# Kernel optimization log

Measured on AMD Instinct MI355X. Metric: run time of the kernel, lower is better.

The kernel has to match this reference:

```python
import jax, jax.numpy as jnp
import numpy as np

N = 50000   # nodes
E = 800000  # edges per relation (avg degree 16)
IN = 128    # input feature dim
H = 2       # attention heads per layer
OUT = 64    # output feats per head
R = 2       # number of relations
NEG_SLOPE = 0.2


def _edge_softmax(e, dst, n):
    # e: [E, H] edge scores; softmax over incoming edges of each dst node
    m = jax.ops.segment_max(e, dst, num_segments=n)  # [N, H]
    m = jnp.where(jnp.isfinite(m), m, 0.0)
    ex = jnp.exp(e - jax.lax.stop_gradient(m)[dst])
    s = jax.ops.segment_sum(ex, dst, num_segments=n)  # [N, H]
    return ex / s[dst]


def _gat_layer(h, W, al, ar, b, src, dst):
    # h: [N, in]; W: [R, in, H*OUT]; al/ar: [R, H, OUT]; b: [R, H*OUT]
    # src/dst: [R, E] int32. HeteroGraphConv with sum aggregation over relations.
    acc = jnp.zeros((N, H, OUT), h.dtype)
    for r in range(R):  # small fixed relation count
        f = (h @ W[r]).reshape(N, H, OUT)           # projected feats
        el = (f * al[r]).sum(-1)                    # [N, H]
        er = (f * ar[r]).sum(-1)                    # [N, H]
        e = jax.nn.leaky_relu(el[src[r]] + er[dst[r]], NEG_SLOPE)  # [E, H]
        a = _edge_softmax(e, dst[r], N)             # [E, H]
        msg = f[src[r]] * a[:, :, None]             # [E, H, OUT]
        agg = jax.ops.segment_sum(msg, dst[r], num_segments=N)     # [N, H, OUT]
        acc = acc + jax.nn.elu(agg + b[r].reshape(1, H, OUT))
    return acc.reshape(N, H * OUT)  # flatten(1)


def setup_inputs() -> dict:
    key = jax.random.key(0)
    k = jax.random.split(key, 13)
    s = 0.05
    f32 = jnp.float32
    return {
        "x": jax.random.normal(k[0], (N, IN), f32),
        "W0": jax.random.normal(k[1], (R, IN, H * OUT), f32) * s,
        "al0": jax.random.normal(k[2], (R, H, OUT), f32) * s,
        "ar0": jax.random.normal(k[3], (R, H, OUT), f32) * s,
        "b0": jax.random.normal(k[4], (R, H * OUT), f32) * s,
        "W1": jax.random.normal(k[5], (R, H * OUT, H * OUT), f32) * s,
        "al1": jax.random.normal(k[6], (R, H, OUT), f32) * s,
        "ar1": jax.random.normal(k[7], (R, H, OUT), f32) * s,
        "b1": jax.random.normal(k[8], (R, H * OUT), f32) * s,
        "src0": jax.random.randint(k[9], (R, E), 0, N, jnp.int32),
        "dst0": jax.random.randint(k[10], (R, E), 0, N, jnp.int32),
        "src1": jax.random.randint(k[11], (R, E), 0, N, jnp.int32),
        "dst1": jax.random.randint(k[12], (R, E), 0, N, jnp.int32),
    }


def reference(x, W0, al0, ar0, b0, W1, al1, ar1, b1, src0, dst0, src1, dst1):
    h = _gat_layer(x, W0, al0, ar0, b0, src0, dst0)  # [N, H*OUT]
    h = _gat_layer(h, W1, al1, ar1, b1, src1, dst1)  # [N, H*OUT]
    return h
```

## Files before the change

kernel.cpp:

```cpp
#include <hip/hip_runtime.h>

#define NN 50000
#define NE 800000
#define DIM 128
#define NB 128
#define CH 4096
#define CAP 8192

typedef unsigned int uint;
typedef unsigned short ushort;
typedef __attribute__((ext_vector_type(8))) short v8s;
typedef __attribute__((ext_vector_type(4))) float v4f;

__device__ __forceinline__ ushort f2bf(float f) {
    union { float f; uint i; } c; c.f = f;
    const uint r = (c.i + 0x7fffu + ((c.i >> 16) & 1u)) >> 16;
    return (ushort)r;
}

__global__ __launch_bounds__(256) void conv_wt(
    const float* __restrict__ W0, const float* __restrict__ W1,
    ushort* __restrict__ WT, int* __restrict__ gcur)
{
    if (blockIdx.x == 64) {
        const int t = threadIdx.x;
        gcur[t] = t * CAP;
        gcur[t + 256] = (t + 256) * CAP;
        return;
    }
    const int t = blockIdx.x * 256 + threadIdx.x;
#pragma unroll
    for (int i = 0; i < 4; i++) {
        const int o = t * 4 + i;
        const int m = o >> 14, rem = o & 16383;
        const int nrow = rem >> 7, k = rem & 127;
        const float* src = (m < 2) ? (W0 + (size_t)m * 16384)
                                   : (W1 + (size_t)(m - 2) * 16384);
        WT[o] = f2bf(src[k * 128 + nrow]);
    }
}

__global__ __launch_bounds__(256) void gemm_dual(
    const ushort* __restrict__ hbf, const float* __restrict__ xf,
    const ushort* __restrict__ WT,
    const float* __restrict__ al, const float* __restrict__ ar,
    ushort* __restrict__ fg0, ushort* __restrict__ fg1,
    float* __restrict__ elb, int n, int is_f32)
{
    __shared__ ushort tile[64][136];
    const int tid = threadIdx.x;
    const int w = tid >> 6, lane = tid & 63;
    const int quad = lane >> 4, l16 = lane & 15;
    const int row0 = blockIdx.x * 64 + w * 16;

    int arow = row0 + l16;
    if (arow >= n) arow = n - 1;

    v8s afr[4];
    if (is_f32) {
        const float* ap = xf + (size_t)arow * DIM + quad * 8;
#pragma unroll
        for (int kt = 0; kt < 4; kt++) {
            const float4 a0 = *(const float4*)(ap + kt * 32);
            const float4 a1 = *(const float4*)(ap + kt * 32 + 4);
            ushort tmp[8] = { f2bf(a0.x), f2bf(a0.y), f2bf(a0.z), f2bf(a0.w),
                              f2bf(a1.x), f2bf(a1.y), f2bf(a1.z), f2bf(a1.w) };
            afr[kt] = *(const v8s*)tmp;
        }
    } else {
        const ushort* ap = hbf + (size_t)arow * DIM + quad * 8;
#pragma unroll
        for (int kt = 0; kt < 4; kt++) afr[kt] = *(const v8s*)(ap + kt * 32);
    }

    for (int rel = 0; rel < 2; rel++) {
        const ushort* bp = WT + (size_t)rel * DIM * DIM + (size_t)l16 * DIM + quad * 8;
        v4f acc[8];
#pragma unroll
        for (int nt = 0; nt < 8; nt++) acc[nt] = (v4f)0.0f;
#pragma unroll
        for (int kt = 0; kt < 4; kt++) {
#pragma unroll
            for (int nt = 0; nt < 8; nt++) {
                const v8s b = *(const v8s*)(bp + (size_t)nt * 16 * DIM + kt * 32);
                acc[nt] = __builtin_amdgcn_mfma_f32_16x16x32_bf16(afr[kt], b, acc[nt], 0, 0, 0);
            }
        }

        const float* alr = al + rel * DIM;
        const float* arr = ar + rel * DIM;
        float pel[4][2], per2[4][2];
#pragma unroll
        for (int r = 0; r < 4; r++)
            pel[r][0] = pel[r][1] = per2[r][0] = per2[r][1] = 0.f;
#pragma unroll
        for (int nt = 0; nt < 8; nt++) {
            const int col = nt * 16 + l16;
            const float av = alr[col], rv = arr[col];
            const int head = nt >> 2;
#pragma unroll
            for (int r = 0; r < 4; r++) {
                pel[r][head] += acc[nt][r] * av;
                per2[r][head] += acc[nt][r] * rv;
            }
        }
#pragma unroll
        for (int o = 1; o < 16; o <<= 1) {
#pragma unroll
            for (int r = 0; r < 4; r++) {
#pragma unroll
                for (int h = 0; h < 2; h++) {
                    pel[r][h] += __shfl_xor(pel[r][h], o);
                    per2[r][h] += __shfl_xor(per2[r][h], o);
                }
            }
        }
        float* elp = elb + (size_t)rel * NN * 4;
        float* erp = elp + (size_t)NN * 2;
        if (l16 == 0) {
#pragma unroll
            for (int r = 0; r < 4; r++) {
                const int row = row0 + quad * 4 + r;
                if (row < n) {
#pragma unroll
                    for (int h = 0; h < 2; h++) {
                        elp[row * 2 + h] = pel[r][h];
                        erp[row * 2 + h] = per2[r][h];
                    }
                }
            }
        }

        __syncthreads();
        const int lr0 = w * 16 + quad * 4;
#pragma unroll
        for (int nt = 0; nt < 8; nt++) {
            const int col = nt * 16 + l16;
#pragma unroll
            for (int r = 0; r < 4; r++)
                tile[lr0 + r][col] = f2bf(acc[nt][r]);
        }
        __syncthreads();
        ushort* fgr = rel ? fg1 : fg0;
        const int srow = tid >> 2, ch = tid & 3;
        const int grow = blockIdx.x * 64 + srow;
        if (grow < n) {
            const uint4* lp = (const uint4*)&tile[srow][ch * 32];
            uint4* gp = (uint4*)(fgr + (size_t)grow * DIM + ch * 32);
            gp[0] = lp[0];
            gp[1] = lp[1];
            gp[2] = lp[2];
            gp[3] = lp[3];
        }
    }
}

__global__ __launch_bounds__(256) void bin_edges(
    const int* __restrict__ dst0, const int* __restrict__ dst1,
    const int* __restrict__ src0, const int* __restrict__ src1,
    int* __restrict__ gcur, uint* __restrict__ binned)
{
    __shared__ int hist[NB], ebase[NB], lcur[NB], gbase[NB], sc[NB];
    __shared__ uint stage[CH];
    const int bpset = (NE + CH - 1) / CH;
    const int bid = blockIdx.x;
    const int s = bid / bpset, cb = bid - s * bpset;
    const int* dstp = (s < 2) ? (dst0 + (size_t)s * NE) : (dst1 + (size_t)(s - 2) * NE);
    const int* srcp = (s < 2) ? (src0 + (size_t)s * NE) : (src1 + (size_t)(s - 2) * NE);
    const int e0 = cb * CH;
    const int t = threadIdx.x;

    if (t < NB) hist[t] = 0;
    __syncthreads();

    int myd[16], mys[16];
#pragma unroll
    for (int k = 0; k < 16; k++) {
        const int e = e0 + t + k * 256;
        if (e < NE) {
            const int d = dstp[e];
            myd[k] = d;
            mys[k] = srcp[e];
            atomicAdd(&hist[(d * NB) / NN], 1);
        } else myd[k] = -1;
    }
    __syncthreads();
    if (t < NB) sc[t] = hist[t];
    __syncthreads();
    for (int o = 1; o < NB; o <<= 1) {
        int tv = 0;
        if (t < NB && t >= o) tv = sc[t - o];
        __syncthreads();
        if (t < NB) sc[t] += tv;
        __syncthreads();
    }
    if (t < NB) {
        ebase[t] = sc[t] - hist[t];
        lcur[t]  = sc[t] - hist[t];
        gbase[t] = atomicAdd(&gcur[s * NB + t], hist[t]);
    }
    __syncthreads();
#pragma unroll
    for (int k = 0; k < 16; k++) {
        if (myd[k] >= 0) {
            const int b = (myd[k] * NB) / NN;
            const int p = atomicAdd(&lcur[b], 1);
            stage[p] = ((uint)myd[k] << 16) | (uint)mys[k];
        }
    }
    __syncthreads();
    const int total = ebase[NB - 1] + hist[NB - 1];
    for (int i = t; i < total; i += 256) {
        const uint v = stage[i];
        const int b = ((int)(v >> 16) * NB) / NN;
        binned[gbase[b] + (i - ebase[b])] = v;
    }
}

__global__ __launch_bounds__(512) void scan_buckets(
    const int* __restrict__ gcur, int* __restrict__ bbase, int* __restrict__ row)
{
    __shared__ int sc[512];
    const int t = threadIdx.x;
    const int s = t >> 7, b = t & (NB - 1);
    const int cnt = gcur[t] - t * CAP;
    sc[t] = cnt;
    __syncthreads();
    for (int o = 1; o < NB; o <<= 1) {
        const int add = (b >= o) ? sc[t - o] : 0;
        __syncthreads();
        sc[t] += add;
        __syncthreads();
    }
    bbase[s * (NB + 1) + b] = sc[t] - cnt;
    if (b == NB - 1) {
        bbase[s * (NB + 1) + NB] = sc[t];
        row[s * (NN + 1) + NN] = NE;
    }
}

__global__ __launch_bounds__(256) void build_csr(
    const int* __restrict__ bbase, const uint* __restrict__ binned,
    int* __restrict__ row, ushort* __restrict__ csr_src)
{
    __shared__ int A[512], B[512], lcur[512];
    const int bid = blockIdx.x;
    const int s = bid >> 7, b = bid & (NB - 1);
    const int nb0 = (b * NN + NB - 1) / NB;
    int nb1 = ((b + 1) * NN + NB - 1) / NB;
    if (nb1 > NN) nb1 = NN;
    const int nloc = nb1 - nb0;
    const int jb = bbase[s * (NB + 1) + b], je = bbase[s * (NB + 1) + b + 1];
    const int cnt = je - jb;
    const uint* bslot = binned + (size_t)(s * NB + b) * CAP;
    const int t = threadIdx.x;

    A[t] = 0; A[t + 256] = 0;
    __syncthreads();
    for (int j = t; j < cnt; j += 256)
        atomicAdd(&A[(int)(bslot[j] >> 16) - nb0], 1);
    __syncthreads();
    const int c0 = A[t], c1 = A[t + 256];
    int* cur = A; int* nxt = B;
    for (int off = 1; off < 512; off <<= 1) {
        nxt[t]       = cur[t]       + ((t >= off)       ? cur[t - off]       : 0);
        nxt[t + 256] = cur[t + 256] + ((t + 256 >= off) ? cur[t + 256 - off] : 0);
        __syncthreads();
        int* tmp = cur; cur = nxt; nxt = tmp;
    }
    if (t < nloc) {
        const int v = jb + cur[t] - c0;
        lcur[t] = v;
        row[s * (NN + 1) + nb0 + t] = v;
    }
    if (t + 256 < nloc) {
        const int v = jb + cur[t + 256] - c1;
        lcur[t + 256] = v;
        row[s * (NN + 1) + nb0 + t + 256] = v;
    }
    __syncthreads();
    ushort* outp = csr_src + (size_t)s * NE;
    for (int j = t; j < cnt; j += 256) {
        const uint v = bslot[j];
        const int p = atomicAdd(&lcur[(int)(v >> 16) - nb0], 1);
        outp[p] = (ushort)(v & 0xffffu);
    }
}

__device__ __forceinline__ float elu(float v) { return v > 0.f ? v : expm1f(v); }
__device__ __forceinline__ float2 bfpair(uint u) {
    union { uint i; float f; } lo, hi;
    lo.i = u << 16;
    hi.i = u & 0xffff0000u;
    return make_float2(lo.f, hi.f);
}

__global__ __launch_bounds__(256) void aggregate_dual(
    const int* __restrict__ row0, const ushort* __restrict__ csr0,
    const int* __restrict__ row1, const ushort* __restrict__ csr1,
    const float2* __restrict__ el0, const float2* __restrict__ er0,
    const float2* __restrict__ el1, const float2* __restrict__ er1,
    const ushort* __restrict__ fg0, const ushort* __restrict__ fg1,
    const float* __restrict__ bias0, const float* __restrict__ bias1,
    float* __restrict__ outf, ushort* __restrict__ outbf, int obf)
{
    __shared__ uint soff[4][64];
    __shared__ float wts[4][2][64];
    const int wv = (blockIdx.x * 256 + threadIdx.x) >> 6;
    if (wv >= NN) return;
    const int lane = threadIdx.x & 63;
    const int wid = threadIdx.x >> 6;

    const int* rows[2] = {row0, row1};
    const ushort* csrs[2] = {csr0, csr1};
    const float2* els[2] = {el0, el1};
    const float2* ers[2] = {er0, er1};
    const ushort* fgs[2] = {fg0, fg1};
    const float* biases[2] = {bias0, bias1};

    float oacc0 = 0.f, oacc1 = 0.f;

#pragma unroll
    for (int rel = 0; rel < 2; rel++) {
        const int beg = rows[rel][wv], end = rows[rel][wv + 1];
        const int deg = end - beg;
        const float2 erd = ers[rel][wv];
        float2 acc = make_float2(0.f, 0.f);

        if (deg <= 64) {
            uint sof = 0;
            float ex0 = 0.f, ex1 = 0.f;
            if (lane < deg) {
                const int s = csrs[rel][beg + lane];
                const float2 e = els[rel][s];
                float e0 = e.x + erd.x, e1 = e.y + erd.y;
                e0 = e0 > 0.f ? e0 : 0.2f * e0;
                e1 = e1 > 0.f ? e1 : 0.2f * e1;
                ex0 = __expf(e0);
                ex1 = __expf(e1);
                sof = (uint)s << 8;
            }
            float den0 = ex0, den1 = ex1;
            for (int o = 32; o > 0; o >>= 1) {
                den0 += __shfl_xor(den0, o);
                den1 += __shfl_xor(den1, o);
            }
            const float inv0 = 1.0f / den0, inv1 = 1.0f / den1;
            soff[wid][lane] = sof;
            wts[wid][0][lane] = ex0 * inv0;
            wts[wid][1][lane] = ex1 * inv1;
            const char* fgb = (const char*)fgs[rel] + lane * 4;
            const float* wrow = wts[wid][lane >> 5];
            const uint* sorow = soff[wid];
            const int dp = (deg + 15) & ~15;
            for (int tt = 0; tt < dp; tt += 16) {
                uint off[16];
                float wgt[16];
#pragma unroll
                for (int k = 0; k < 16; k++) {
                    off[k] = sorow[tt + k];
                    wgt[k] = wrow[tt + k];
                }
                uint u[16];
#pragma unroll
                for (int k = 0; k < 16; k++)
                    u[k] = *(const uint*)(fgb + off[k]);
#pragma unroll
                for (int k = 0; k < 16; k++) {
                    const float2 f = bfpair(u[k]);
                    acc.x += f.x * wgt[k];
                    acc.y += f.y * wgt[k];
                }
            }
        } else {
            float den0 = 0.f, den1 = 0.f;
            for (int c0 = beg; c0 < end; c0 += 64) {
                const int j = c0 + lane;
                if (j < end) {
                    const float2 e = els[rel][csrs[rel][j]];
                    float e0 = e.x + erd.x, e1 = e.y + erd.y;
                    e0 = e0 > 0.f ? e0 : 0.2f * e0;
                    e1 = e1 > 0.f ? e1 : 0.2f * e1;
                    den0 += __expf(e0);
                    den1 += __expf(e1);
                }
            }
            for (int o = 32; o > 0; o >>= 1) {
                den0 += __shfl_xor(den0, o);
                den1 += __shfl_xor(den1, o);
            }
            const float inv0 = 1.0f / den0, inv1 = 1.0f / den1;
            for (int c0 = beg; c0 < end; c0 += 64) {
                const int j = c0 + lane;
                int s = -1;
                float ex0 = 0.f, ex1 = 0.f;
                if (j < end) {
                    s = csrs[rel][j];
                    const float2 e = els[rel][s];
                    float e0 = e.x + erd.x, e1 = e.y + erd.y;
                    e0 = e0 > 0.f ? e0 : 0.2f * e0;
                    e1 = e1 > 0.f ? e1 : 0.2f * e1;
                    ex0 = __expf(e0) * inv0;
                    ex1 = __expf(e1) * inv1;
                }
                const int cm = min(64, end - c0);
                for (int tt = 0; tt < cm; tt++) {
                    const int st = __shfl(s, tt);
                    const float a0 = __shfl(ex0, tt);
                    const float a1 = __shfl(ex1, tt);
                    const float aa = (lane < 32) ? a0 : a1;
                    const float2 fv = bfpair(
                        *(const uint*)((const char*)fgs[rel] + ((size_t)st << 8) + lane * 4));
                    acc.x += fv.x * aa;
                    acc.y += fv.y * aa;
                }
            }
        }

        const float b0 = biases[rel][2 * lane], b1 = biases[rel][2 * lane + 1];
        oacc0 += elu(acc.x + b0);
        oacc1 += elu(acc.y + b1);
    }

    if (obf) {
        ushort tmp[2] = { f2bf(oacc0), f2bf(oacc1) };
        *(uint*)(outbf + (size_t)wv * DIM + 2 * lane) = *(const uint*)tmp;
    } else {
        float* op = outf + (size_t)wv * DIM + 2 * lane;
        op[0] = oacc0; op[1] = oacc1;
    }
}

extern "C" void kernel_launch(void* const* d_in, const int* in_sizes, int n_in,
                              void* d_out, int out_size, void* d_ws, size_t ws_size,
                              hipStream_t stream)
{
    const float* x   = (const float*)d_in[0];
    const float* W0  = (const float*)d_in[1];
    const float* al0 = (const float*)d_in[2];
    const float* ar0 = (const float*)d_in[3];
    const float* b0  = (const float*)d_in[4];
    const float* W1  = (const float*)d_in[5];
    const float* al1 = (const float*)d_in[6];
    const float* ar1 = (const float*)d_in[7];
    const float* b1  = (const float*)d_in[8];
    const int* src0 = (const int*)d_in[9];
    const int* dst0 = (const int*)d_in[10];
    const int* src1 = (const int*)d_in[11];
    const int* dst1 = (const int*)d_in[12];
    float* out = (float*)d_out;

    char* w = (char*)d_ws;
    auto alloc = [&](size_t bytes) {
        char* p = w; w += (bytes + 255) & ~(size_t)255; return p;
    };
    ushort* h1bf   = (ushort*)alloc((size_t)NN * DIM * 2);
    ushort* fg0    = (ushort*)alloc((size_t)NN * DIM * 2);
    ushort* fg1    = (ushort*)alloc((size_t)NN * DIM * 2);
    ushort* WT     = (ushort*)alloc((size_t)4 * DIM * DIM * 2);
    float*  elb    = (float*)alloc((size_t)8 * NN * 4);
    int*    row    = (int*)alloc((size_t)4 * (NN + 1) * 4);
    ushort* csr    = (ushort*)alloc((size_t)4 * NE * 2);
    uint*   binned = (uint*)alloc((size_t)4 * NB * CAP * 4);
    int*    bbase  = (int*)alloc((size_t)4 * (NB + 1) * 4);
    int*    gcur   = (int*)alloc((size_t)4 * NB * 4);

    conv_wt<<<65, 256, 0, stream>>>(W0, W1, WT, gcur);
    {
        const int bpset = (NE + CH - 1) / CH;
        bin_edges<<<4 * bpset, 256, 0, stream>>>(dst0, dst1, src0, src1, gcur, binned);
    }
    scan_buckets<<<1, 512, 0, stream>>>(gcur, bbase, row);
    build_csr<<<4 * NB, 256, 0, stream>>>(bbase, binned, row, csr);

    const int gblocks = (NN + 63) / 64;
    for (int L = 0; L < 2; L++) {
        const ushort* WTl = WT + (size_t)L * 2 * DIM * DIM;
        const float* al  = L ? al1 : al0;
        const float* ar  = L ? ar1 : ar0;
        const float* b   = L ? b1 : b0;
        gemm_dual<<<gblocks, 256, 0, stream>>>(
            L ? h1bf : nullptr, L ? nullptr : x, WTl, al, ar,
            fg0, fg1, elb, NN, L ? 0 : 1);
        const int es0 = L * 2, es1 = L * 2 + 1;
        float* el0p = elb;
        float* er0p = elb + (size_t)NN * 2;
        float* el1p = elb + (size_t)NN * 4;
        float* er1p = elb + (size_t)NN * 6;
        aggregate_dual<<<(NN * 64 + 255) / 256, 256, 0, stream>>>(
            row + es0 * (NN + 1), csr + (size_t)es0 * NE,
            row + es1 * (NN + 1), csr + (size_t)es1 * NE,
            (const float2*)el0p, (const float2*)er0p,
            (const float2*)el1p, (const float2*)er1p,
            fg0, fg1, b, b + DIM,
            L ? out : nullptr, L ? nullptr : h1bf, L ? 0 : 1);
    }
}
```

Baseline: 355.1 us.

## Fuse edge binning with layer-0 GEMM and fold bucket scan into CSR build

Layer-0 projection GEMM blocks and edge-binning blocks now run in one heterogeneous launch that shares a single shared-memory buffer, overlapping two independent workloads. The separate single-block bucket scan kernel is removed, and each build_csr block recomputes the prefix over bucket counts itself. This cuts launch count and serialization between prep stages, at the cost of redundant scan work per CSR block and a larger fused kernel.

```diff
diff --git a/kernel.cpp b/kernel.cpp
--- a/kernel.cpp
+++ b/kernel.cpp
@@ -6,6 +6,8 @@
 #define NB 128
 #define CH 4096
 #define CAP 8192
+#define BPSET ((NE + CH - 1) / CH)
+#define NBIN_BLOCKS (4 * BPSET)
 
 typedef unsigned int uint;
 typedef unsigned short ushort;
@@ -40,18 +42,18 @@
     }
 }
 
-__global__ __launch_bounds__(256) void gemm_dual(
+__device__ __forceinline__ void gemm_body(
+    ushort (*tile)[136],
     const ushort* __restrict__ hbf, const float* __restrict__ xf,
     const ushort* __restrict__ WT,
     const float* __restrict__ al, const float* __restrict__ ar,
     ushort* __restrict__ fg0, ushort* __restrict__ fg1,
-    float* __restrict__ elb, int n, int is_f32)
-{
-    __shared__ ushort tile[64][136];
+    float* __restrict__ elb, int n, int is_f32, int bid)
+{
     const int tid = threadIdx.x;
     const int w = tid >> 6, lane = tid & 63;
     const int quad = lane >> 4, l16 = lane & 15;
-    const int row0 = blockIdx.x * 64 + w * 16;
+    const int row0 = bid * 64 + w * 16;
 
     int arow = row0 + l16;
     if (arow >= n) arow = n - 1;
@@ -143,7 +145,7 @@
         __syncthreads();
         ushort* fgr = rel ? fg1 : fg0;
         const int srow = tid >> 2, ch = tid & 3;
-        const int grow = blockIdx.x * 64 + srow;
+        const int grow = bid * 64 + srow;
         if (grow < n) {
             const uint4* lp = (const uint4*)&tile[srow][ch * 32];
             uint4* gp = (uint4*)(fgr + (size_t)grow * DIM + ch * 32);
@@ -155,16 +157,31 @@
     }
 }
 
-__global__ __launch_bounds__(256) void bin_edges(
+__global__ __launch_bounds__(256) void gemm_dual(
+    const ushort* __restrict__ hbf, const float* __restrict__ xf,
+    const ushort* __restrict__ WT,
+    const float* __restrict__ al, const float* __restrict__ ar,
+    ushort* __restrict__ fg0, ushort* __restrict__ fg1,
+    float* __restrict__ elb, int n, int is_f32)
+{
+    __shared__ ushort tile[64][136];
+    gemm_body(tile, hbf, xf, WT, al, ar, fg0, fg1, elb, n, is_f32, blockIdx.x);
+}
+
+__device__ __forceinline__ void bin_body(
+    char* smem,
     const int* __restrict__ dst0, const int* __restrict__ dst1,
     const int* __restrict__ src0, const int* __restrict__ src1,
-    int* __restrict__ gcur, uint* __restrict__ binned)
-{
-    __shared__ int hist[NB], ebase[NB], lcur[NB], gbase[NB], sc[NB];
-    __shared__ uint stage[CH];
-    const int bpset = (NE + CH - 1) / CH;
-    const int bid = blockIdx.x;
-    const int s = bid / bpset, cb = bid - s * bpset;
+    int* __restrict__ gcur, uint* __restrict__ binned, int bid)
+{
+    int* hist  = (int*)smem;
+    int* ebase = hist + NB;
+    int* lcur  = ebase + NB;
+    int* gbase = lcur + NB;
+    int* sc    = gbase + NB;
+    uint* stage = (uint*)(sc + NB);
+
+    const int s = bid / BPSET, cb = bid - s * BPSET;
     const int* dstp = (s < 2) ? (dst0 + (size_t)s * NE) : (dst1 + (size_t)(s - 2) * NE);
     const int* srcp = (s < 2) ? (src0 + (size_t)s * NE) : (src1 + (size_t)(s - 2) * NE);
     const int e0 = cb * CH;
@@ -217,43 +234,54 @@
     }
 }
 
-__global__ __launch_bounds__(512) void scan_buckets(
-    const int* __restrict__ gcur, int* __restrict__ bbase, int* __restrict__ row)
-{
-    __shared__ int sc[512];
-    const int t = threadIdx.x;
-    const int s = t >> 7, b = t & (NB - 1);
-    const int cnt = gcur[t] - t * CAP;
-    sc[t] = cnt;
-    __syncthreads();
-    for (int o = 1; o < NB; o <<= 1) {
-        const int add = (b >= o) ? sc[t - o] : 0;
-        __syncthreads();
-        sc[t] += add;
-        __syncthreads();
-    }
-    bbase[s * (NB + 1) + b] = sc[t] - cnt;
-    if (b == NB - 1) {
-        bbase[s * (NB + 1) + NB] = sc[t];
-        row[s * (NN + 1) + NN] = NE;
+__global__ __launch_bounds__(256) void prep_fused(
+    const int* __restrict__ dst0, const int* __restrict__ dst1,
+    const int* __restrict__ src0, const int* __restrict__ src1,
+    int* __restrict__ gcur, uint* __restrict__ binned,
+    const float* __restrict__ xf, const ushort* __restrict__ WT,
+    const float* __restrict__ al, const float* __restrict__ ar,
+    ushort* __restrict__ fg0, ushort* __restrict__ fg1,
+    float* __restrict__ elb)
+{
+    __shared__ __align__(16) char smem[18944];
+    const int bid = blockIdx.x;
+    if (bid < NBIN_BLOCKS) {
+        bin_body(smem, dst0, dst1, src0, src1, gcur, binned, bid);
+    } else {
+        gemm_body((ushort(*)[136])smem, nullptr, xf, WT, al, ar,
+                  fg0, fg1, elb, NN, 1, bid - NBIN_BLOCKS);
     }
 }
 
 __global__ __launch_bounds__(256) void build_csr(
-    const int* __restrict__ bbase, const uint* __restrict__ binned,
+    const int* __restrict__ gcur, const uint* __restrict__ binned,
     int* __restrict__ row, ushort* __restrict__ csr_src)
 {
     __shared__ int A[512], B[512], lcur[512];
+    __shared__ int pfx[NB + 1];
     const int bid = blockIdx.x;
     const int s = bid >> 7, b = bid & (NB - 1);
+    const int t = threadIdx.x;
+
+    if (t < NB) pfx[t + 1] = gcur[s * NB + t] - (s * NB + t) * CAP;
+    if (t == 0) pfx[0] = 0;
+    __syncthreads();
+    for (int o = 1; o < NB; o <<= 1) {
+        int v = 0;
+        if (t < NB && t >= o) v = pfx[t - o + 1];
+        __syncthreads();
+        if (t < NB) pfx[t + 1] += v;
+        __syncthreads();
+    }
+    const int jb = pfx[b], je = pfx[b + 1];
+    const int cnt = je - jb;
+    if (b == NB - 1 && t == 0) row[s * (NN + 1) + NN] = NE;
+
     const int nb0 = (b * NN + NB - 1) / NB;
     int nb1 = ((b + 1) * NN + NB - 1) / NB;
     if (nb1 > NN) nb1 = NN;
     const int nloc = nb1 - nb0;
-    const int jb = bbase[s * (NB + 1) + b], je = bbase[s * (NB + 1) + b + 1];
-    const int cnt = je - jb;
     const uint* bslot = binned + (size_t)(s * NB + b) * CAP;
-    const int t = threadIdx.x;
 
     A[t] = 0; A[t + 256] = 0;
     __syncthreads();
@@ -462,26 +490,22 @@
     int*    row    = (int*)alloc((size_t)4 * (NN + 1) * 4);
     ushort* csr    = (ushort*)alloc((size_t)4 * NE * 2);
     uint*   binned = (uint*)alloc((size_t)4 * NB * CAP * 4);
-    int*    bbase  = (int*)alloc((size_t)4 * (NB + 1) * 4);
     int*    gcur   = (int*)alloc((size_t)4 * NB * 4);
 
     conv_wt<<<65, 256, 0, stream>>>(W0, W1, WT, gcur);
-    {
-        const int bpset = (NE + CH - 1) / CH;
-        bin_edges<<<4 * bpset, 256, 0, stream>>>(dst0, dst1, src0, src1, gcur, binned);
-    }
-    scan_buckets<<<1, 512, 0, stream>>>(gcur, bbase, row);
-    build_csr<<<4 * NB, 256, 0, stream>>>(bbase, binned, row, csr);
+    prep_fused<<<NBIN_BLOCKS + (NN + 63) / 64, 256, 0, stream>>>(
+        dst0, dst1, src0, src1, gcur, binned,
+        x, WT, al0, ar0, fg0, fg1, elb);
+    build_csr<<<4 * NB, 256, 0, stream>>>(gcur, binned, row, csr);
 
     const int gblocks = (NN + 63) / 64;
     for (int L = 0; L < 2; L++) {
-        const ushort* WTl = WT + (size_t)L * 2 * DIM * DIM;
-        const float* al  = L ? al1 : al0;
-        const float* ar  = L ? ar1 : ar0;
-        const float* b   = L ? b1 : b0;
-        gemm_dual<<<gblocks, 256, 0, stream>>>(
-            L ? h1bf : nullptr, L ? nullptr : x, WTl, al, ar,
-            fg0, fg1, elb, NN, L ? 0 : 1);
+        if (L) {
+            gemm_dual<<<gblocks, 256, 0, stream>>>(
+                h1bf, nullptr, WT + (size_t)2 * DIM * DIM, al1, ar1,
+                fg0, fg1, elb, NN, 0);
+        }
+        const float* b = L ? b1 : b0;
         const int es0 = L * 2, es1 = L * 2 + 1;
         float* el0p = elb;
         float* er0p = elb + (size_t)NN * 2;
```

New measurement: 346.1 us. -2.5%, faster.
